# Performance work log

Hardware: AMD Instinct MI355X
Metric: run time of the kernel (lower is better)

## Reference

```python
import jax, jax.numpy as jnp
import numpy as np

SHARED_DIM = 512
ENC_IN = 512
LATENT = 16
BATCH = 65536
NUM_CLASSES = 16


def setup_inputs() -> dict:
    key = jax.random.key(0)
    ks = jax.random.split(key, 12)
    s = 1.0 / np.sqrt(SHARED_DIM)
    si = 1.0 / np.sqrt(ENC_IN)
    return {
        "x": jax.random.normal(ks[0], (BATCH, ENC_IN), dtype=jnp.float32),
        # shared MLP: two ReLU hiddens + identity output (rlkit Mlp)
        "W0": jax.random.uniform(ks[1], (SHARED_DIM, ENC_IN), jnp.float32, -si, si),
        "b0": jnp.zeros((SHARED_DIM,), jnp.float32),
        "W1": jax.random.uniform(ks[2], (SHARED_DIM, SHARED_DIM), jnp.float32, -s, s),
        "b1": jnp.zeros((SHARED_DIM,), jnp.float32),
        "W2": jax.random.uniform(ks[3], (SHARED_DIM, SHARED_DIM), jnp.float32, -s, s),
        "b2": jnp.zeros((SHARED_DIM,), jnp.float32),
        # class encoder (router)
        "Wc": jax.random.uniform(ks[4], (NUM_CLASSES, SHARED_DIM), jnp.float32, -s, s),
        "bc": jnp.zeros((NUM_CLASSES,), jnp.float32),
        # per-class gaussian experts, stacked: [K, 2*latent, shared_dim]
        "Wg": jax.random.uniform(ks[5], (NUM_CLASSES, 2 * LATENT, SHARED_DIM), jnp.float32, -s, s),
        "bg": jnp.zeros((NUM_CLASSES, 2 * LATENT), jnp.float32),
    }


def reference(x, W0, b0, W1, b1, W2, b2, Wc, bc, Wg, bg):
    # shared encoder: ReLU MLP with identity output layer
    m = jax.nn.relu(x @ W0.T + b0)
    m = jax.nn.relu(m @ W1.T + b1)
    m = m @ W2.T + b2                      # [B, D]
    # router: softmax over classes, then most-likely class per sample
    y_probs = jax.nn.softmax(m @ Wc.T + bc, axis=-1)   # [B, K]
    y = jnp.argmax(y_probs, axis=1)                    # [B]
    # evaluate ALL per-class experts densely (as the original does)
    mu_sigma = jnp.einsum('bd,ked->bke', m, Wg) + bg   # [B, K, 2L]
    mu = mu_sigma[..., :LATENT]                        # Normal mean; sampler='mean'
    # gather the selected class's mean per sample
    z = jnp.take_along_axis(mu, y[:, None, None], axis=1)[:, 0, :]  # [B, L]
    return (z, y)
```

## Files before the change

### kernel.cpp

```cpp
#include <hip/hip_runtime.h>
#include <hip/hip_bf16.h>

typedef __attribute__((ext_vector_type(8))) short short8;
typedef __attribute__((ext_vector_type(16))) float floatx16;
typedef __attribute__((ext_vector_type(4))) float floatx4;

#define AS1 __attribute__((address_space(1)))
#define AS3 __attribute__((address_space(3)))

constexpr int MM = 65536;
constexpr int KK = 512;
constexpr int NN = 512;

#define GM 128
#define GN 128
#define GK 32
#define LDT 40

__device__ __forceinline__ unsigned short bf16_rn(float v) {
  unsigned u = __float_as_uint(v);
  return (unsigned short)((u + 0x7FFFu + ((u >> 16) & 1u)) >> 16);
}
__device__ __forceinline__ float bf16_to_f32(unsigned short h) {
  return __uint_as_float((unsigned)h << 16);
}

__global__ __launch_bounds__(256) void split_kernel(
    const float* __restrict__ src, unsigned short* __restrict__ h,
    unsigned short* __restrict__ l, int n4) {
  int i = blockIdx.x * 256 + threadIdx.x;
  if (i >= n4) return;
  float4 v = ((const float4*)src)[i];
  ushort4 hv, lv;
  hv.x = bf16_rn(v.x); lv.x = bf16_rn(v.x - bf16_to_f32(hv.x));
  hv.y = bf16_rn(v.y); lv.y = bf16_rn(v.y - bf16_to_f32(hv.y));
  hv.z = bf16_rn(v.z); lv.z = bf16_rn(v.z - bf16_to_f32(hv.z));
  hv.w = bf16_rn(v.w); lv.w = bf16_rn(v.w - bf16_to_f32(hv.w));
  ((ushort4*)h)[i] = hv;
  ((ushort4*)l)[i] = lv;
}

template<bool RELU>
__global__ __launch_bounds__(512, 1) void gemm_mfma(
    const unsigned short* __restrict__ Ah, const unsigned short* __restrict__ Al,
    const unsigned short* __restrict__ Wh, const unsigned short* __restrict__ Wl,
    const float* __restrict__ bias,
    unsigned short* __restrict__ Ch, unsigned short* __restrict__ Cl) {
  __shared__ __align__(16) unsigned short smem[65536];
  const int tid = threadIdx.x;
  const int lane = tid & 63;
  const int wid = tid >> 6;
  const int wr = wid >> 2;
  const int wc = wid & 3;
  const int nwg = gridDim.x;
  const int hw  = blockIdx.x;
  const int logical = (hw & 7) * (nwg >> 3) + (hw >> 3);
  const int bm = logical >> 1, bn = logical & 1;
  const size_t Abase = (size_t)bm * 256 * KK;
  const size_t Bbase = (size_t)bn * 256 * KK;

  const int sarr  = wid >> 1;
  const int rbase = (wid & 1) * 128;
  const unsigned short* gsrc = (sarr == 0) ? Ah : (sarr == 1) ? Al
                             : (sarr == 2) ? Wh : Wl;
  const size_t tb = (sarr < 2) ? Abase : Bbase;
  const int rowl = lane >> 2;
  const int gch  = (lane & 3) ^ ((lane >> 3) & 3);
  const unsigned short* gbase = gsrc + tb + (size_t)(rbase + rowl) * KK + gch * 8;
  unsigned short* ldst = smem + sarr * 8192 + rbase * 32;

  auto stage = [&](int buf, int kk) {
#pragma unroll
    for (int j = 0; j < 8; ++j) {
      __builtin_amdgcn_global_load_lds(
          (const AS1 unsigned int*)(gbase + (size_t)(j * 16) * KK + kk),
          (AS3 unsigned int*)(ldst + buf * 32768 + j * 16 * 32),
          16, 0, 0);
    }
  };

  floatx16 acc[4][2];
#pragma unroll
  for (int i = 0; i < 4; ++i)
#pragma unroll
    for (int j = 0; j < 2; ++j)
#pragma unroll
      for (int r = 0; r < 16; ++r) acc[i][j][r] = 0.f;

  stage(0, 0);

  const int swz = (lane >> 1) & 3;
  int cur = 0;
#pragma unroll
  for (int t = 0; t < 16; ++t) {
    if (t < 15) {
      stage(cur ^ 1, (t + 1) * GK);
      asm volatile("s_waitcnt vmcnt(8)" ::: "memory");
    } else {
      asm volatile("s_waitcnt vmcnt(0)" ::: "memory");
    }
    __builtin_amdgcn_s_barrier();
    __builtin_amdgcn_sched_barrier(0);

    const unsigned short* base = smem + cur * 32768;
#pragma unroll
    for (int ks = 0; ks < 2; ++ks) {
      const int ch = ks * 2 + (lane >> 5);
      const int sw = (ch ^ swz) * 8;
      short8 fah[4], fal[4], fbh[2], fbl[2];
#pragma unroll
      for (int ri = 0; ri < 4; ++ri) {
        int row = wr * 128 + ri * 32 + (lane & 31);
        fah[ri] = *(const short8*)(base + row * 32 + sw);
        fal[ri] = *(const short8*)(base + 8192 + row * 32 + sw);
      }
#pragma unroll
      for (int si = 0; si < 2; ++si) {
        int col = wc * 64 + si * 32 + (lane & 31);
        fbh[si] = *(const short8*)(base + 16384 + col * 32 + sw);
        fbl[si] = *(const short8*)(base + 24576 + col * 32 + sw);
      }
      __builtin_amdgcn_s_setprio(1);
#pragma unroll
      for (int ri = 0; ri < 4; ++ri)
#pragma unroll
        for (int si = 0; si < 2; ++si) {
          acc[ri][si] = __builtin_amdgcn_mfma_f32_32x32x16_bf16(fah[ri], fbh[si], acc[ri][si], 0, 0, 0);
          acc[ri][si] = __builtin_amdgcn_mfma_f32_32x32x16_bf16(fah[ri], fbl[si], acc[ri][si], 0, 0, 0);
          acc[ri][si] = __builtin_amdgcn_mfma_f32_32x32x16_bf16(fal[ri], fbh[si], acc[ri][si], 0, 0, 0);
        }
      __builtin_amdgcn_s_setprio(0);
    }
    __builtin_amdgcn_sched_barrier(0);
    __builtin_amdgcn_s_barrier();
    cur ^= 1;
  }

  float bv[2];
#pragma unroll
  for (int si = 0; si < 2; ++si)
    bv[si] = bias[bn * 256 + wc * 64 + si * 32 + (lane & 31)];

  unsigned* lds32 = (unsigned*)smem;
#pragma unroll
  for (int ri = 0; ri < 4; ++ri) {
    __syncthreads();
#pragma unroll
    for (int si = 0; si < 2; ++si) {
      int lcol = wc * 64 + si * 32 + (lane & 31);
#pragma unroll
      for (int r = 0; r < 16; ++r) {
        int frow = (r & 3) + 8 * (r >> 2) + 4 * (lane >> 5);
        float v = acc[ri][si][r] + bv[si];
        if (RELU) v = fmaxf(v, 0.f);
        unsigned short h = bf16_rn(v);
        unsigned short lo = bf16_rn(v - bf16_to_f32(h));
        lds32[(wr * 32 + frow) * 256 + lcol] = (unsigned)h | ((unsigned)lo << 16);
      }
    }
    __syncthreads();
#pragma unroll
    for (int p = 0; p < 8; ++p) {
      int c = tid + p * 512;
      int lrow = c >> 6;
      int cc = (c & 63) * 4;
      uint4 d = *(const uint4*)&lds32[lrow * 256 + cc];
      ushort4 hv, lv;
      hv.x = (unsigned short)(d.x); lv.x = (unsigned short)(d.x >> 16);
      hv.y = (unsigned short)(d.y); lv.y = (unsigned short)(d.y >> 16);
      hv.z = (unsigned short)(d.z); lv.z = (unsigned short)(d.z >> 16);
      hv.w = (unsigned short)(d.w); lv.w = (unsigned short)(d.w >> 16);
      int grow = bm * 256 + (lrow >> 5) * 128 + ri * 32 + (lrow & 31);
      size_t gi = (size_t)grow * NN + bn * 256 + cc;
      *(ushort4*)&Ch[gi] = hv;
      *(ushort4*)&Cl[gi] = lv;
    }
  }
}

__global__ __launch_bounds__(256, 2) void gemm_muz(
    const unsigned short* __restrict__ Ahm, const unsigned short* __restrict__ Wh,
    const float* __restrict__ bias, const float* __restrict__ y_in,
    float* __restrict__ z_out) {
  __shared__ __align__(16) unsigned short smem[16384];
  unsigned short* sA = smem;
  unsigned short* sB = smem + 8192;
  const int tid = threadIdx.x;
  const int lane = tid & 63;
  const int wid = tid >> 6;
  const int wr = wid >> 1;
  const int wc = wid & 1;
  const int nwg = gridDim.x;
  const int hw  = blockIdx.x;
  const int logical = (hw & 7) * (nwg >> 3) + (hw >> 3);
  const int bm = logical >> 1, bn = logical & 1;
  const size_t Abase = (size_t)bm * GM * KK;
  const size_t Bbase = (size_t)bn * GN * KK;

  const unsigned short* gsrc = (wid < 2) ? Ahm : Wh;
  const size_t tb = (wid < 2) ? Abase : Bbase;
  unsigned short* ldst = (wid < 2) ? sA : sB;
  const int rbase = (wid & 1) * 64;
  const int rowl = lane >> 2;
  const int gch  = (lane & 3) ^ ((lane >> 3) & 3);
  const unsigned short* gbase = gsrc + tb + (size_t)rowl * KK + gch * 8;

  auto stage = [&](int buf, int kk) {
#pragma unroll
    for (int j = 0; j < 4; ++j) {
      const int r0 = rbase + j * 16;
      __builtin_amdgcn_global_load_lds(
          (const AS1 unsigned int*)(gbase + (size_t)r0 * KK + kk),
          (AS3 unsigned int*)(ldst + buf * 4096 + r0 * GK),
          16, 0, 0);
    }
  };

  floatx16 acc[2][2];
#pragma unroll
  for (int i = 0; i < 2; ++i)
#pragma unroll
    for (int j = 0; j < 2; ++j)
#pragma unroll
      for (int r = 0; r < 16; ++r) acc[i][j][r] = 0.f;

  stage(0, 0);

  const int swz = (lane >> 1) & 3;
  int cur = 0;
#pragma unroll
  for (int k0 = 0; k0 < KK; k0 += GK) {
    if (k0 + GK < KK) {
      stage(cur ^ 1, k0 + GK);
      asm volatile("s_waitcnt vmcnt(4)" ::: "memory");
    } else {
      asm volatile("s_waitcnt vmcnt(0)" ::: "memory");
    }
    __builtin_amdgcn_s_barrier();
    __builtin_amdgcn_sched_barrier(0);

    const unsigned short* pA = sA + cur * 4096;
    const unsigned short* pB = sB + cur * 4096;
#pragma unroll
    for (int ks = 0; ks < 2; ++ks) {
      const int ch = ks * 2 + (lane >> 5);
      const int sw = (ch ^ swz) * 8;
      short8 fa[2], fb[2];
#pragma unroll
      for (int ri = 0; ri < 2; ++ri) {
        int row = wr * 64 + ri * 32 + (lane & 31);
        fa[ri] = *(const short8*)(pA + row * GK + sw);
      }
#pragma unroll
      for (int si = 0; si < 2; ++si) {
        int col = wc * 64 + si * 32 + (lane & 31);
        fb[si] = *(const short8*)(pB + col * GK + sw);
      }
#pragma unroll
      for (int ri = 0; ri < 2; ++ri)
#pragma unroll
        for (int si = 0; si < 2; ++si)
          acc[ri][si] = __builtin_amdgcn_mfma_f32_32x32x16_bf16(fa[ri], fb[si], acc[ri][si], 0, 0, 0);
    }
    __builtin_amdgcn_sched_barrier(0);
    __builtin_amdgcn_s_barrier();
    cur ^= 1;
  }

  int colv[2]; float bv[2];
#pragma unroll
  for (int si = 0; si < 2; ++si) {
    colv[si] = bn * GN + wc * 64 + si * 32 + (lane & 31);
    bv[si] = bias[colv[si]];
  }
#pragma unroll
  for (int ri = 0; ri < 2; ++ri)
#pragma unroll
    for (int r = 0; r < 16; ++r) {
      int row = bm * GM + wr * 64 + ri * 32 + (r & 3) + 8 * (r >> 2) + 4 * (lane >> 5);
      int yv = (int)y_in[row];
#pragma unroll
      for (int si = 0; si < 2; ++si) {
        if ((colv[si] >> 4) == yv)
          z_out[(size_t)row * 16 + (colv[si] & 15)] = acc[ri][si][r] + bv[si];
      }
    }
}

__global__ __launch_bounds__(256) void logits_kernel(
    const unsigned short* __restrict__ mh, const unsigned short* __restrict__ ml,
    const unsigned short* __restrict__ wch, const unsigned short* __restrict__ wcl,
    const float* __restrict__ bc, float* __restrict__ y_out) {
  __shared__ unsigned short smh[64][LDT], sml[64][LDT];
  __shared__ float slog[64][17];
  const int tid = threadIdx.x;
  const int lane = tid & 63;
  const int wid = tid >> 6;
  const size_t row0 = (size_t)blockIdx.x * 64;
  const int fr = lane & 15;
  const int fq = lane >> 4;

  floatx4 acc = {0.f, 0.f, 0.f, 0.f};
  const unsigned short* bh = wch + fr * 512 + fq * 8;
  const unsigned short* bl = wcl + fr * 512 + fq * 8;

  for (int k0 = 0; k0 < 512; k0 += 32) {
    {
      int row = tid >> 2, cc = (tid & 3) * 8;
      size_t g = (row0 + row) * 512 + k0 + cc;
      *(short8*)&smh[row][cc] = *(const short8*)(mh + g);
      *(short8*)&sml[row][cc] = *(const short8*)(ml + g);
    }
    __syncthreads();
    short8 ah = *(const short8*)&smh[wid * 16 + fr][fq * 8];
    short8 al = *(const short8*)&sml[wid * 16 + fr][fq * 8];
    short8 fbh = *(const short8*)(bh + k0);
    short8 fbl = *(const short8*)(bl + k0);
    acc = __builtin_amdgcn_mfma_f32_16x16x32_bf16(ah, fbh, acc, 0, 0, 0);
    acc = __builtin_amdgcn_mfma_f32_16x16x32_bf16(ah, fbl, acc, 0, 0, 0);
    acc = __builtin_amdgcn_mfma_f32_16x16x32_bf16(al, fbh, acc, 0, 0, 0);
    __syncthreads();
  }
#pragma unroll
  for (int r = 0; r < 4; ++r)
    slog[wid * 16 + fq * 4 + r][fr] = acc[r] + bc[fr];
  __syncthreads();
  if (tid < 64) {
    float best = slog[tid][0];
    int bi = 0;
#pragma unroll
    for (int j = 1; j < 16; ++j) {
      float v = slog[tid][j];
      if (v > best) { best = v; bi = j; }
    }
    y_out[row0 + tid] = (float)bi;
  }
}

__global__ __launch_bounds__(256) void prep_wg(
    const float* __restrict__ Wg, const float* __restrict__ bg,
    unsigned short* __restrict__ wgh, float* __restrict__ wgb) {
  int gid = blockIdx.x * 256 + threadIdx.x;
  if (gid >= 32768) return;
  int r = gid >> 7;
  int c4 = (gid & 127) * 4;
  int k = r >> 4, e = r & 15;
  float4 v = *(const float4*)(Wg + ((size_t)k * 32 + e) * 512 + c4);
  ushort4 h;
  h.x = bf16_rn(v.x); h.y = bf16_rn(v.y); h.z = bf16_rn(v.z); h.w = bf16_rn(v.w);
  *(ushort4*)(wgh + (size_t)r * 512 + c4) = h;
  if (c4 == 0) wgb[r] = bg[k * 32 + e];
}

extern "C" void kernel_launch(void* const* d_in, const int* in_sizes, int n_in,
                              void* d_out, int out_size, void* d_ws, size_t ws_size,
                              hipStream_t stream) {
  const float* x  = (const float*)d_in[0];
  const float* W0 = (const float*)d_in[1];
  const float* b0 = (const float*)d_in[2];
  const float* W1 = (const float*)d_in[3];
  const float* b1 = (const float*)d_in[4];
  const float* W2 = (const float*)d_in[5];
  const float* b2 = (const float*)d_in[6];
  const float* Wc = (const float*)d_in[7];
  const float* bc = (const float*)d_in[8];
  const float* Wg = (const float*)d_in[9];
  const float* bg = (const float*)d_in[10];

  const size_t NEL = (size_t)MM * KK;
  unsigned short* Ah = (unsigned short*)d_ws;
  unsigned short* Al = Ah + NEL;
  unsigned short* Bh = Al + NEL;
  unsigned short* Bl = Bh + NEL;
  unsigned short* wch = Al;
  unsigned short* wcl = Al + 8192;
  unsigned short* wgh = Al + 16384;
  float* wgb = (float*)(Al + 16384 + 131072);

  unsigned short* w0h = (unsigned short*)d_out;
  unsigned short* w0l = w0h + 262144;
  unsigned short* w1h = w0l + 262144;
  unsigned short* w1l = w1h + 262144;
  unsigned short* w2h = w1l + 262144;
  unsigned short* w2l = w2h + 262144;

  float* z_out = (float*)d_out;
  float* y_out = z_out + (size_t)MM * 16;

  split_kernel<<<(int)(NEL / 4 / 256), 256, 0, stream>>>(x, Ah, Al, (int)(NEL / 4));
  split_kernel<<<256, 256, 0, stream>>>(W0, w0h, w0l, 65536);
  split_kernel<<<256, 256, 0, stream>>>(W1, w1h, w1l, 65536);
  split_kernel<<<256, 256, 0, stream>>>(W2, w2h, w2l, 65536);

  const int ngrid = (MM / 256) * (NN / 256);
  gemm_mfma<true ><<<ngrid, 512, 0, stream>>>(Ah, Al, w0h, w0l, b0, Bh, Bl);
  gemm_mfma<true ><<<ngrid, 512, 0, stream>>>(Bh, Bl, w1h, w1l, b1, Ah, Al);
  gemm_mfma<false><<<ngrid, 512, 0, stream>>>(Ah, Al, w2h, w2l, b2, Bh, Bl);

  split_kernel<<<8, 256, 0, stream>>>(Wc, wch, wcl, 2048);
  prep_wg<<<128, 256, 0, stream>>>(Wg, bg, wgh, wgb);

  logits_kernel<<<MM / 64, 256, 0, stream>>>(Bh, Bl, wch, wcl, bc, y_out);
  gemm_muz<<<(MM / GM) * 2, 256, 0, stream>>>(Bh, wgh, wgb, y_out, z_out);
}
```

Measured before the change: 624.2 us.

## Interleave next-tile global-to-LDS staging with MFMA phases in GEMM main loop

Splits each K-step of the GEMM main loop into four compute phases, each covering half the A rows for one 16-wide K sub-slice. The global_load_lds prefetch of the next tile is split into four pieces, one issued per phase, rather than one burst at the start of the step. The goal is to spread memory traffic across the MFMA work and to hold fewer A fragments in registers at once. The cost is several extra workgroup barriers per K-step, which can stall waves, and a tighter vmcnt wait.

```diff
diff --git a/kernel.cpp b/kernel.cpp
--- a/kernel.cpp
+++ b/kernel.cpp
@@ -69,9 +69,9 @@
   const unsigned short* gbase = gsrc + tb + (size_t)(rbase + rowl) * KK + gch * 8;
   unsigned short* ldst = smem + sarr * 8192 + rbase * 32;
 
-  auto stage = [&](int buf, int kk) {
-#pragma unroll
-    for (int j = 0; j < 8; ++j) {
+  auto stage2 = [&](int buf, int kk, int p) {
+#pragma unroll
+    for (int j = p * 2; j < p * 2 + 2; ++j) {
       __builtin_amdgcn_global_load_lds(
           (const AS1 unsigned int*)(gbase + (size_t)(j * 16) * KK + kk),
           (AS3 unsigned int*)(ldst + buf * 32768 + j * 16 * 32),
@@ -87,53 +87,69 @@
 #pragma unroll
       for (int r = 0; r < 16; ++r) acc[i][j][r] = 0.f;
 
-  stage(0, 0);
+#pragma unroll
+  for (int p = 0; p < 4; ++p) stage2(0, 0, p);
 
   const int swz = (lane >> 1) & 3;
-  int cur = 0;
 #pragma unroll
   for (int t = 0; t < 16; ++t) {
-    if (t < 15) {
-      stage(cur ^ 1, (t + 1) * GK);
-      asm volatile("s_waitcnt vmcnt(8)" ::: "memory");
-    } else {
-      asm volatile("s_waitcnt vmcnt(0)" ::: "memory");
-    }
-    __builtin_amdgcn_s_barrier();
-    __builtin_amdgcn_sched_barrier(0);
-
+    const int cur = t & 1;
     const unsigned short* base = smem + cur * 32768;
-#pragma unroll
-    for (int ks = 0; ks < 2; ++ks) {
+    short8 fbh[2], fbl[2];
+#pragma unroll
+    for (int p = 0; p < 4; ++p) {
+      const int ks = p >> 1, h = p & 1;
       const int ch = ks * 2 + (lane >> 5);
       const int sw = (ch ^ swz) * 8;
-      short8 fah[4], fal[4], fbh[2], fbl[2];
-#pragma unroll
-      for (int ri = 0; ri < 4; ++ri) {
-        int row = wr * 128 + ri * 32 + (lane & 31);
-        fah[ri] = *(const short8*)(base + row * 32 + sw);
-        fal[ri] = *(const short8*)(base + 8192 + row * 32 + sw);
-      }
-#pragma unroll
-      for (int si = 0; si < 2; ++si) {
-        int col = wc * 64 + si * 32 + (lane & 31);
-        fbh[si] = *(const short8*)(base + 16384 + col * 32 + sw);
-        fbl[si] = *(const short8*)(base + 24576 + col * 32 + sw);
-      }
+      short8 fah[2], fal[2];
+
+      if (p == 0) {
+        if (t < 15) {
+          stage2(cur ^ 1, (t + 1) * GK, 0);
+          asm volatile("s_waitcnt vmcnt(2)" ::: "memory");
+        } else {
+          asm volatile("s_waitcnt vmcnt(0)" ::: "memory");
+        }
+        __builtin_amdgcn_s_barrier();
+        __builtin_amdgcn_sched_barrier(0);
+      }
+
+#pragma unroll
+      for (int q = 0; q < 2; ++q) {
+        int row = wr * 128 + (h * 2 + q) * 32 + (lane & 31);
+        fah[q] = *(const short8*)(base + row * 32 + sw);
+        fal[q] = *(const short8*)(base + 8192 + row * 32 + sw);
+      }
+      if (h == 0) {
+#pragma unroll
+        for (int si = 0; si < 2; ++si) {
+          int col = wc * 64 + si * 32 + (lane & 31);
+          fbh[si] = *(const short8*)(base + 16384 + col * 32 + sw);
+          fbl[si] = *(const short8*)(base + 24576 + col * 32 + sw);
+        }
+      }
+
+      if (p > 0) {
+        if (t < 15) stage2(cur ^ 1, (t + 1) * GK, p);
+        __builtin_amdgcn_sched_barrier(0);
+        __builtin_amdgcn_s_barrier();
+        __builtin_amdgcn_sched_barrier(0);
+      }
+
       __builtin_amdgcn_s_setprio(1);
 #pragma unroll
-      for (int ri = 0; ri < 4; ++ri)
+      for (int q = 0; q < 2; ++q)
 #pragma unroll
         for (int si = 0; si < 2; ++si) {
-          acc[ri][si] = __builtin_amdgcn_mfma_f32_32x32x16_bf16(fah[ri], fbh[si], acc[ri][si], 0, 0, 0);
-          acc[ri][si] = __builtin_amdgcn_mfma_f32_32x32x16_bf16(fah[ri], fbl[si], acc[ri][si], 0, 0, 0);
-          acc[ri][si] = __builtin_amdgcn_mfma_f32_32x32x16_bf16(fal[ri], fbh[si], acc[ri][si], 0, 0, 0);
+          const int ri = h * 2 + q;
+          acc[ri][si] = __builtin_amdgcn_mfma_f32_32x32x16_bf16(fah[q], fbh[si], acc[ri][si], 0, 0, 0);
+          acc[ri][si] = __builtin_amdgcn_mfma_f32_32x32x16_bf16(fah[q], fbl[si], acc[ri][si], 0, 0, 0);
+          acc[ri][si] = __builtin_amdgcn_mfma_f32_32x32x16_bf16(fal[q], fbh[si], acc[ri][si], 0, 0, 0);
         }
       __builtin_amdgcn_s_setprio(0);
-    }
-    __builtin_amdgcn_sched_barrier(0);
-    __builtin_amdgcn_s_barrier();
-    cur ^= 1;
+      __builtin_amdgcn_sched_barrier(0);
+      __builtin_amdgcn_s_barrier();
+    }
   }
 
   float bv[2];
```

Result: no change. 615.5 us (-1.4%).
